# Kernel tuning notes

Measured on AMD Instinct MI355X. Metric: run time of the kernel, lower is better.

## Reference

```python
import jax, jax.numpy as jnp
import numpy as np

WINDOW_SIZE = 512  # init kwarg

def setup_inputs() -> dict:
    key = jax.random.key(0)
    kq, kk, kv = jax.random.split(key, 3)
    B, H, S, D = 1, 16, 4096, 64
    q = jax.random.normal(kq, (B, H, S, D), dtype=jnp.float32)
    k = jax.random.normal(kk, (B, H, S, D), dtype=jnp.float32)
    v = jax.random.normal(kv, (B, H, S, D), dtype=jnp.float32)
    return {"q": q, "k": k, "v": v}

def reference(q, k, v):
    # q,k,v: [B, H, S, D]
    B, H, S, D = q.shape
    scale = 1.0 / jnp.sqrt(jnp.asarray(D, dtype=q.dtype))
    scores = jnp.einsum('bhqd,bhkd->bhqk', q, k) * scale  # [B,H,S,S]
    # sliding-window band mask: token i attends to j in [i - w//2, i + w//2]
    idx = jnp.arange(S)
    band = jnp.abs(idx[:, None] - idx[None, :]) <= (WINDOW_SIZE // 2)  # [S,S]
    scores = jnp.where(band, scores, -jnp.inf)  # same as adding -inf mask
    probs = jax.nn.softmax(scores, axis=-1)
    return jnp.einsum('bhqk,bhkd->bhqd', probs, v)
```

## Files before the change

### kernel.cpp

```cpp
#include <hip/hip_runtime.h>
#include <math.h>

#define SEQ   4096
#define HD    64
#define NH    16
#define WHALF 256
#define QB    128
#define KT    64
#define KSTR  72
#define PLANE (KT * KSTR)

typedef __attribute__((ext_vector_type(8))) __bf16 bf16x8;
typedef __attribute__((ext_vector_type(8))) short short8v;
typedef __attribute__((ext_vector_type(4))) float f32x4;

__device__ __forceinline__ short bf16bits(float x) {
    __bf16 b = (__bf16)x;
    return __builtin_bit_cast(short, b);
}

#define MFMA32(A, B, C) __builtin_amdgcn_mfma_f32_16x16x32_bf16((A), (B), (C), 0, 0, 0)

#if __has_builtin(__builtin_amdgcn_exp2f)
#define EXP2F(x) __builtin_amdgcn_exp2f(x)
#else
#define EXP2F(x) __exp2f(x)
#endif

__global__ __launch_bounds__(512, 4)
void swa_mfma7_kernel(const float* __restrict__ q,
                      const float* __restrict__ k,
                      const float* __restrict__ v,
                      float* __restrict__ out) {
    __shared__ short smem[2 * 2 * PLANE];
    __shared__ short onesP[16 * KSTR];

    const int orig = blockIdx.x;
    const int work = ((orig & 7) << 6) + (orig >> 3);
    const int h    = work >> 5;
    const int q0   = (work & 31) * QB;

    const int t    = threadIdx.x;
    const int lane = t & 63;
    const int w    = t >> 6;
    const int n15  = lane & 15;
    const int g    = lane >> 4;
    const int qrow = q0 + w * 16 + n15;

    const float SCALE = 0.125f * 1.44269504088896340736f;

    for (int idx = t; idx < 16 * KSTR; idx += 512)
        onesP[idx] = (idx < KSTR) ? (short)0x3F80 : (short)0;

    bf16x8 qf[2];
    {
        const float* qp = q + ((size_t)h * SEQ + qrow) * HD;
        #pragma unroll
        for (int c = 0; c < 2; ++c) {
            const float4* p4 = reinterpret_cast<const float4*>(qp + 32 * c + 8 * g);
            float4 a = p4[0], b = p4[1];
            float xs[8] = {a.x, a.y, a.z, a.w, b.x, b.y, b.z, b.w};
            short8v q8;
            #pragma unroll
            for (int j = 0; j < 8; ++j) q8[j] = bf16bits(xs[j] * SCALE);
            qf[c] = __builtin_bit_cast(bf16x8, q8);
        }
    }

    f32x4 accO[4];
    #pragma unroll
    for (int dt = 0; dt < 4; ++dt) accO[dt] = (f32x4){0.f, 0.f, 0.f, 0.f};
    f32x4 accL = (f32x4){0.f, 0.f, 0.f, 0.f};

    int k0 = q0 - WHALF;           if (k0 < 0) k0 = 0;
    int k1 = q0 + QB - 1 + WHALF;  if (k1 > SEQ - 1) k1 = SEQ - 1;
    const int nt = (k1 + 1 - k0) >> 6;

    const int wqmin = q0 + w * 16;
    const int wqmax = wqmin + 15;
    const int wlo   = wqmin - WHALF;
    const int whi   = wqmax + WHALF;

    const float4* kb4 = reinterpret_cast<const float4*>(k + ((size_t)h * SEQ) * HD);
    const float*  vp  = v + ((size_t)h * SEQ) * HD;

    float4 kreg[2];
    float  vreg[8];

    #define LOADT(KTV)                                                       \
        {                                                                    \
            const int kt_ = (KTV);                                           \
            kreg[0] = kb4[(size_t)kt_ * 16 + t * 2 + 0];                     \
            kreg[1] = kb4[(size_t)kt_ * 16 + t * 2 + 1];                     \
            _Pragma("unroll")                                                \
            for (int j = 0; j < 8; ++j)                                      \
                vreg[j] = vp[(size_t)(kt_ + 8 * w + j) * HD + lane];         \
        }

    auto STAGE = [&](int b) {
        short* Kb = smem + b * 2 * PLANE;
        short* Vb = Kb + PLANE;

        const int p  = t >> 3;
        const int q5 = p & 31;
        const int R  = (p & 32) + (((q5 >> 2) & 1) << 4) + ((q5 >> 3) << 2) + (q5 & 3);

        const float* kf = reinterpret_cast<const float*>(&kreg[0]);
        short8v k8;
        #pragma unroll
        for (int j = 0; j < 8; ++j) k8[j] = bf16bits(kf[j]);
        *reinterpret_cast<short8v*>(&Kb[R * KSTR + (t & 7) * 8]) = k8;

        short8v v8;
        #pragma unroll
        for (int j = 0; j < 8; ++j) v8[j] = bf16bits(vreg[j]);
        *reinterpret_cast<short8v*>(&Vb[lane * KSTR + 8 * w]) = v8;
    };

    LOADT(k0);
    STAGE(0);
    if (nt > 1) LOADT(k0 + KT);
    __syncthreads();

    for (int i = 0; i < nt; ++i) {
        const int kt  = k0 + i * KT;
        const int cur = i & 1;

        if (i + 1 < nt) {
            STAGE(cur ^ 1);
            if (i + 2 < nt) LOADT(k0 + (i + 2) * KT);
        }

        const short* Kb = smem + cur * 2 * PLANE;
        const short* Vb = Kb + PLANE;

        #pragma unroll
        for (int kc = 0; kc < 2; ++kc) {
            const int cb = kt + kc * 32;
            if (cb > whi || cb + 31 < wlo) continue;

            f32x4 S[2];
            __builtin_amdgcn_s_setprio(1);
            #pragma unroll
            for (int s = 0; s < 2; ++s) {
                const int krow = (kc * 32 + s * 16 + n15) * KSTR + 8 * g;
                bf16x8 k0f = __builtin_bit_cast(bf16x8, *reinterpret_cast<const short8v*>(&Kb[krow]));
                bf16x8 k1f = __builtin_bit_cast(bf16x8, *reinterpret_cast<const short8v*>(&Kb[krow + 32]));
                f32x4 a = (f32x4){0.f, 0.f, 0.f, 0.f};
                a = MFMA32(k0f, qf[0], a);
                a = MFMA32(k1f, qf[1], a);
                S[s] = a;
            }
            __builtin_amdgcn_s_setprio(0);

            short8v p8s;
            const bool interior = (cb >= wqmax - WHALF) && (cb + 31 <= wqmin + WHALF);
            if (interior) {
                #pragma unroll
                for (int j = 0; j < 8; ++j)
                    p8s[j] = bf16bits(EXP2F(S[j >> 2][j & 3]));
            } else {
                const int kbase = cb + 8 * g;
                #pragma unroll
                for (int j = 0; j < 8; ++j) {
                    int key = kbase + j;
                    bool valid = (key >= qrow - WHALF) && (key <= qrow + WHALF);
                    float x = valid ? S[j >> 2][j & 3] : -1e30f;
                    p8s[j] = bf16bits(EXP2F(x));
                }
            }
            bf16x8 p8 = __builtin_bit_cast(bf16x8, p8s);

            __builtin_amdgcn_s_setprio(1);
            #pragma unroll
            for (int dt = 0; dt < 4; ++dt) {
                const int vrow = (dt * 16 + n15) * KSTR + kc * 32 + 8 * g;
                bf16x8 vf = __builtin_bit_cast(bf16x8, *reinterpret_cast<const short8v*>(&Vb[vrow]));
                accO[dt] = MFMA32(vf, p8, accO[dt]);
            }
            {
                bf16x8 of = __builtin_bit_cast(bf16x8,
                    *reinterpret_cast<const short8v*>(&onesP[n15 * KSTR + kc * 32 + 8 * g]));
                accL = MFMA32(of, p8, accL);
            }
            __builtin_amdgcn_s_setprio(0);
        }

        if (i + 1 < nt) __syncthreads();
    }

    const float lsum = __shfl(accL[0], n15);
    const float inv  = 1.0f / lsum;
    float* op = out + ((size_t)h * SEQ + qrow) * HD;
    #pragma unroll
    for (int dt = 0; dt < 4; ++dt) {
        *reinterpret_cast<f32x4*>(op + dt * 16 + 4 * g) = accO[dt] * inv;
    }
}

extern "C" void kernel_launch(void* const* d_in, const int* in_sizes, int n_in,
                              void* d_out, int out_size, void* d_ws, size_t ws_size,
                              hipStream_t stream) {
    const float* q = (const float*)d_in[0];
    const float* k = (const float*)d_in[1];
    const float* v = (const float*)d_in[2];
    float* out = (float*)d_out;

    dim3 grid(NH * (SEQ / QB));
    dim3 block(512);
    hipLaunchKernelGGL(swa_mfma7_kernel, grid, block, 0, stream, q, k, v, out);
}
```

Baseline: 27.97 us.

## Double query tile per block so each wave reuses K/V fragments for two row groups

```diff
diff --git a/kernel.cpp b/kernel.cpp
--- a/kernel.cpp
+++ b/kernel.cpp
@@ -5,7 +5,7 @@
 #define HD    64
 #define NH    16
 #define WHALF 256
-#define QB    128
+#define QB    256
 #define KT    64
 #define KSTR  72
 #define PLANE (KT * KSTR)
@@ -27,59 +27,73 @@
 #define EXP2F(x) __exp2f(x)
 #endif
 
-__global__ __launch_bounds__(512, 4)
-void swa_mfma7_kernel(const float* __restrict__ q,
+__global__ __launch_bounds__(512, 2)
+void swa_mfma8_kernel(const float* __restrict__ q,
                       const float* __restrict__ k,
                       const float* __restrict__ v,
                       float* __restrict__ out) {
     __shared__ short smem[2 * 2 * PLANE];
-    __shared__ short onesP[16 * KSTR];
 
     const int orig = blockIdx.x;
-    const int work = ((orig & 7) << 6) + (orig >> 3);
-    const int h    = work >> 5;
-    const int q0   = (work & 31) * QB;
+    const int work = ((orig & 7) << 5) | (orig >> 3);
+    const int h    = work >> 4;
+    const int q0   = (work & 15) * QB;
 
     const int t    = threadIdx.x;
     const int lane = t & 63;
     const int w    = t >> 6;
     const int n15  = lane & 15;
     const int g    = lane >> 4;
-    const int qrow = q0 + w * 16 + n15;
+
+    const int qa      = q0 + w * 32;
+    const int qrow_a  = qa + n15;
+    const int qrow_b  = qa + 16 + n15;
 
     const float SCALE = 0.125f * 1.44269504088896340736f;
 
-    for (int idx = t; idx < 16 * KSTR; idx += 512)
-        onesP[idx] = (idx < KSTR) ? (short)0x3F80 : (short)0;
-
-    bf16x8 qf[2];
+    bf16x8 qfa[2], qfb[2];
     {
-        const float* qp = q + ((size_t)h * SEQ + qrow) * HD;
+        const float* qpa = q + ((size_t)h * SEQ + qrow_a) * HD;
+        const float* qpb = q + ((size_t)h * SEQ + qrow_b) * HD;
         #pragma unroll
         for (int c = 0; c < 2; ++c) {
-            const float4* p4 = reinterpret_cast<const float4*>(qp + 32 * c + 8 * g);
-            float4 a = p4[0], b = p4[1];
-            float xs[8] = {a.x, a.y, a.z, a.w, b.x, b.y, b.z, b.w};
-            short8v q8;
+            const float4* pa4 = reinterpret_cast<const float4*>(qpa + 32 * c + 8 * g);
+            const float4* pb4 = reinterpret_cast<const float4*>(qpb + 32 * c + 8 * g);
+            float4 a0 = pa4[0], a1 = pa4[1], b0 = pb4[0], b1 = pb4[1];
+            float xa[8] = {a0.x, a0.y, a0.z, a0.w, a1.x, a1.y, a1.z, a1.w};
+            float xb[8] = {b0.x, b0.y, b0.z, b0.w, b1.x, b1.y, b1.z, b1.w};
+            short8v qa8, qb8;
             #pragma unroll
-            for (int j = 0; j < 8; ++j) q8[j] = bf16bits(xs[j] * SCALE);
-            qf[c] = __builtin_bit_cast(bf16x8, q8);
-        }
-    }
-
-    f32x4 accO[4];
+            for (int j = 0; j < 8; ++j) {
+                qa8[j] = bf16bits(xa[j] * SCALE);
+                qb8[j] = bf16bits(xb[j] * SCALE);
+            }
+            qfa[c] = __builtin_bit_cast(bf16x8, qa8);
+            qfb[c] = __builtin_bit_cast(bf16x8, qb8);
+        }
+    }
+
+    bf16x8 ones8;
+    {
+        short8v o8;
+        const short ov = (n15 == 0) ? (short)0x3F80 : (short)0;
+        #pragma unroll
+        for (int j = 0; j < 8; ++j) o8[j] = ov;
+        ones8 = __builtin_bit_cast(bf16x8, o8);
+    }
+
+    f32x4 accOa[4], accOb[4];
     #pragma unroll
-    for (int dt = 0; dt < 4; ++dt) accO[dt] = (f32x4){0.f, 0.f, 0.f, 0.f};
-    f32x4 accL = (f32x4){0.f, 0.f, 0.f, 0.f};
+    for (int dt = 0; dt < 4; ++dt) {
+        accOa[dt] = (f32x4){0.f, 0.f, 0.f, 0.f};
+        accOb[dt] = (f32x4){0.f, 0.f, 0.f, 0.f};
+    }
+    f32x4 accLa = (f32x4){0.f, 0.f, 0.f, 0.f};
+    f32x4 accLb = (f32x4){0.f, 0.f, 0.f, 0.f};
 
     int k0 = q0 - WHALF;           if (k0 < 0) k0 = 0;
     int k1 = q0 + QB - 1 + WHALF;  if (k1 > SEQ - 1) k1 = SEQ - 1;
     const int nt = (k1 + 1 - k0) >> 6;
-
-    const int wqmin = q0 + w * 16;
-    const int wqmax = wqmin + 15;
-    const int wlo   = wqmin - WHALF;
-    const int whi   = wqmax + WHALF;
 
     const float4* kb4 = reinterpret_cast<const float4*>(k + ((size_t)h * SEQ) * HD);
     const float*  vp  = v + ((size_t)h * SEQ) * HD;
@@ -137,64 +151,95 @@
         #pragma unroll
         for (int kc = 0; kc < 2; ++kc) {
             const int cb = kt + kc * 32;
-            if (cb > whi || cb + 31 < wlo) continue;
-
-            f32x4 S[2];
+            const bool aact = !(cb > qa + 15 + WHALF || cb + 31 < qa - WHALF);
+            const bool bact = !(cb > qa + 31 + WHALF || cb + 31 < qa + 16 - WHALF);
+            if (!aact && !bact) continue;
+
+            f32x4 Sa[2], Sb[2];
             __builtin_amdgcn_s_setprio(1);
             #pragma unroll
             for (int s = 0; s < 2; ++s) {
                 const int krow = (kc * 32 + s * 16 + n15) * KSTR + 8 * g;
                 bf16x8 k0f = __builtin_bit_cast(bf16x8, *reinterpret_cast<const short8v*>(&Kb[krow]));
                 bf16x8 k1f = __builtin_bit_cast(bf16x8, *reinterpret_cast<const short8v*>(&Kb[krow + 32]));
-                f32x4 a = (f32x4){0.f, 0.f, 0.f, 0.f};
-                a = MFMA32(k0f, qf[0], a);
-                a = MFMA32(k1f, qf[1], a);
-                S[s] = a;
+                if (aact) {
+                    f32x4 a = (f32x4){0.f, 0.f, 0.f, 0.f};
+                    a = MFMA32(k0f, qfa[0], a);
+                    a = MFMA32(k1f, qfa[1], a);
+                    Sa[s] = a;
+                }
+                if (bact) {
+                    f32x4 b = (f32x4){0.f, 0.f, 0.f, 0.f};
+                    b = MFMA32(k0f, qfb[0], b);
+                    b = MFMA32(k1f, qfb[1], b);
+                    Sb[s] = b;
+                }
             }
             __builtin_amdgcn_s_setprio(0);
 
-            short8v p8s;
-            const bool interior = (cb >= wqmax - WHALF) && (cb + 31 <= wqmin + WHALF);
-            if (interior) {
-                #pragma unroll
-                for (int j = 0; j < 8; ++j)
-                    p8s[j] = bf16bits(EXP2F(S[j >> 2][j & 3]));
-            } else {
-                const int kbase = cb + 8 * g;
-                #pragma unroll
-                for (int j = 0; j < 8; ++j) {
-                    int key = kbase + j;
-                    bool valid = (key >= qrow - WHALF) && (key <= qrow + WHALF);
-                    float x = valid ? S[j >> 2][j & 3] : -1e30f;
-                    p8s[j] = bf16bits(EXP2F(x));
-                }
-            }
-            bf16x8 p8 = __builtin_bit_cast(bf16x8, p8s);
+            const int kbase = cb + 8 * g;
+            bf16x8 pa8, pb8;
+            if (aact) {
+                short8v p8s;
+                const bool interior = (cb >= qa + 15 - WHALF) && (cb + 31 <= qa + WHALF);
+                if (interior) {
+                    #pragma unroll
+                    for (int j = 0; j < 8; ++j)
+                        p8s[j] = bf16bits(EXP2F(Sa[j >> 2][j & 3]));
+                } else {
+                    #pragma unroll
+                    for (int j = 0; j < 8; ++j) {
+                        int key = kbase + j;
+                        bool valid = (key >= qrow_a - WHALF) && (key <= qrow_a + WHALF);
+                        p8s[j] = bf16bits(EXP2F(valid ? Sa[j >> 2][j & 3] : -1e30f));
+                    }
+                }
+                pa8 = __builtin_bit_cast(bf16x8, p8s);
+            }
+            if (bact) {
+                short8v p8s;
+                const bool interior = (cb >= qa + 31 - WHALF) && (cb + 31 <= qa + 16 + WHALF);
+                if (interior) {
+                    #pragma unroll
+                    for (int j = 0; j < 8; ++j)
+                        p8s[j] = bf16bits(EXP2F(Sb[j >> 2][j & 3]));
+                } else {
+                    #pragma unroll
+                    for (int j = 0; j < 8; ++j) {
+                        int key = kbase + j;
+                        bool valid = (key >= qrow_b - WHALF) && (key <= qrow_b + WHALF);
+                        p8s[j] = bf16bits(EXP2F(valid ? Sb[j >> 2][j & 3] : -1e30f));
+                    }
+                }
+                pb8 = __builtin_bit_cast(bf16x8, p8s);
+            }
 
             __builtin_amdgcn_s_setprio(1);
             #pragma unroll
             for (int dt = 0; dt < 4; ++dt) {
                 const int vrow = (dt * 16 + n15) * KSTR + kc * 32 + 8 * g;
                 bf16x8 vf = __builtin_bit_cast(bf16x8, *reinterpret_cast<const short8v*>(&Vb[vrow]));
-                accO[dt] = MFMA32(vf, p8, accO[dt]);
-            }
-            {
-                bf16x8 of = __builtin_bit_cast(bf16x8,
-                    *reinterpret_cast<const short8v*>(&onesP[n15 * KSTR + kc * 32 + 8 * g]));
-                accL = MFMA32(of, p8, accL);
-            }
+                if (aact) accOa[dt] = MFMA32(vf, pa8, accOa[dt]);
+                if (bact) accOb[dt] = MFMA32(vf, pb8, accOb[dt]);
+            }
+            if (aact) accLa = MFMA32(ones8, pa8, accLa);
+            if (bact) accLb = MFMA32(ones8, pb8, accLb);
             __builtin_amdgcn_s_setprio(0);
         }
 
         if (i + 1 < nt) __syncthreads();
     }
 
-    const float lsum = __shfl(accL[0], n15);
-    const float inv  = 1.0f / lsum;
-    float* op = out + ((size_t)h * SEQ + qrow) * HD;
+    const float lsa = __shfl(accLa[0], n15);
+    const float lsb = __shfl(accLb[0], n15);
+    const float inva = 1.0f / lsa;
+    const float invb = 1.0f / lsb;
+    float* opa = out + ((size_t)h * SEQ + qrow_a) * HD;
+    float* opb = out + ((size_t)h * SEQ + qrow_b) * HD;
     #pragma unroll
     for (int dt = 0; dt < 4; ++dt) {
-        *reinterpret_cast<f32x4*>(op + dt * 16 + 4 * g) = accO[dt] * inv;
+        *reinterpret_cast<f32x4*>(opa + dt * 16 + 4 * g) = accOa[dt] * inva;
+        *reinterpret_cast<f32x4*>(opb + dt * 16 + 4 * g) = accOb[dt] * invb;
     }
 }
 
@@ -208,5 +253,5 @@
 
     dim3 grid(NH * (SEQ / QB));
     dim3 block(512);
-    hipLaunchKernelGGL(swa_mfma7_kernel, grid, block, 0, stream, q, k, v, out);
+    hipLaunchKernelGGL(swa_mfma8_kernel, grid, block, 0, stream, q, k, v, out);
 }
```

Result: slower. 33.05 us (+18.2%).

## Double key tile to 128 rows and keep ones-vector for row sums in registers

Applied to the files above, without the earlier changes.

```diff
diff --git a/kernel.cpp b/kernel.cpp
--- a/kernel.cpp
+++ b/kernel.cpp
@@ -6,9 +6,12 @@
 #define NH    16
 #define WHALF 256
 #define QB    128
-#define KT    64
+#define KT    128
 #define KSTR  72
-#define PLANE (KT * KSTR)
+#define VSTR  136
+#define KPLANE (KT * KSTR)
+#define VPLANE (HD * VSTR)
+#define BUFSZ  (KPLANE + VPLANE)
 
 typedef __attribute__((ext_vector_type(8))) __bf16 bf16x8;
 typedef __attribute__((ext_vector_type(8))) short short8v;
@@ -28,12 +31,11 @@
 #endif
 
 __global__ __launch_bounds__(512, 4)
-void swa_mfma7_kernel(const float* __restrict__ q,
-                      const float* __restrict__ k,
-                      const float* __restrict__ v,
-                      float* __restrict__ out) {
-    __shared__ short smem[2 * 2 * PLANE];
-    __shared__ short onesP[16 * KSTR];
+void swa_mfma10_kernel(const float* __restrict__ q,
+                       const float* __restrict__ k,
+                       const float* __restrict__ v,
+                       float* __restrict__ out) {
+    __shared__ short smem[2 * BUFSZ];
 
     const int orig = blockIdx.x;
     const int work = ((orig & 7) << 6) + (orig >> 3);
@@ -48,9 +50,6 @@
     const int qrow = q0 + w * 16 + n15;
 
     const float SCALE = 0.125f * 1.44269504088896340736f;
-
-    for (int idx = t; idx < 16 * KSTR; idx += 512)
-        onesP[idx] = (idx < KSTR) ? (short)0x3F80 : (short)0;
 
     bf16x8 qf[2];
     {
@@ -67,6 +66,15 @@
         }
     }
 
+    bf16x8 ones8;
+    {
+        short8v o8;
+        const short ov = (n15 == 0) ? (short)0x3F80 : (short)0;
+        #pragma unroll
+        for (int j = 0; j < 8; ++j) o8[j] = ov;
+        ones8 = __builtin_bit_cast(bf16x8, o8);
+    }
+
     f32x4 accO[4];
     #pragma unroll
     for (int dt = 0; dt < 4; ++dt) accO[dt] = (f32x4){0.f, 0.f, 0.f, 0.f};
@@ -74,7 +82,7 @@
 
     int k0 = q0 - WHALF;           if (k0 < 0) k0 = 0;
     int k1 = q0 + QB - 1 + WHALF;  if (k1 > SEQ - 1) k1 = SEQ - 1;
-    const int nt = (k1 + 1 - k0) >> 6;
+    const int nt = (k1 + 1 - k0) >> 7;
 
     const int wqmin = q0 + w * 16;
     const int wqmax = wqmin + 15;
@@ -84,37 +92,46 @@
     const float4* kb4 = reinterpret_cast<const float4*>(k + ((size_t)h * SEQ) * HD);
     const float*  vp  = v + ((size_t)h * SEQ) * HD;
 
-    float4 kreg[2];
-    float  vreg[8];
-
-    #define LOADT(KTV)                                                       \
-        {                                                                    \
-            const int kt_ = (KTV);                                           \
-            kreg[0] = kb4[(size_t)kt_ * 16 + t * 2 + 0];                     \
-            kreg[1] = kb4[(size_t)kt_ * 16 + t * 2 + 1];                     \
-            _Pragma("unroll")                                                \
-            for (int j = 0; j < 8; ++j)                                      \
-                vreg[j] = vp[(size_t)(kt_ + 8 * w + j) * HD + lane];         \
+    float4 kreg[4];
+    float  vreg[16];
+
+    #define LOADT(KTV)                                                        \
+        {                                                                     \
+            const int kt_ = (KTV);                                            \
+            _Pragma("unroll")                                                 \
+            for (int i = 0; i < 4; ++i)                                       \
+                kreg[i] = kb4[(size_t)kt_ * 16 + t * 4 + i];                  \
+            _Pragma("unroll")                                                 \
+            for (int j = 0; j < 16; ++j)                                      \
+                vreg[j] = vp[(size_t)(kt_ + 16 * w + j) * HD + lane];         \
         }
 
     auto STAGE = [&](int b) {
-        short* Kb = smem + b * 2 * PLANE;
-        short* Vb = Kb + PLANE;
-
-        const int p  = t >> 3;
+        short* Kb = smem + b * BUFSZ;
+        short* Vb = Kb + KPLANE;
+
+        const int p  = t >> 2;
         const int q5 = p & 31;
-        const int R  = (p & 32) + (((q5 >> 2) & 1) << 4) + ((q5 >> 3) << 2) + (q5 & 3);
+        const int R  = (p & 96) + (((q5 >> 2) & 1) << 4) + ((q5 >> 3) << 2) + (q5 & 3);
 
         const float* kf = reinterpret_cast<const float*>(&kreg[0]);
-        short8v k8;
-        #pragma unroll
-        for (int j = 0; j < 8; ++j) k8[j] = bf16bits(kf[j]);
-        *reinterpret_cast<short8v*>(&Kb[R * KSTR + (t & 7) * 8]) = k8;
-
-        short8v v8;
-        #pragma unroll
-        for (int j = 0; j < 8; ++j) v8[j] = bf16bits(vreg[j]);
-        *reinterpret_cast<short8v*>(&Vb[lane * KSTR + 8 * w]) = v8;
+        short8v k8a, k8b;
+        #pragma unroll
+        for (int j = 0; j < 8; ++j) {
+            k8a[j] = bf16bits(kf[j]);
+            k8b[j] = bf16bits(kf[8 + j]);
+        }
+        *reinterpret_cast<short8v*>(&Kb[R * KSTR + (t & 3) * 16])     = k8a;
+        *reinterpret_cast<short8v*>(&Kb[R * KSTR + (t & 3) * 16 + 8]) = k8b;
+
+        short8v v8a, v8b;
+        #pragma unroll
+        for (int j = 0; j < 8; ++j) {
+            v8a[j] = bf16bits(vreg[j]);
+            v8b[j] = bf16bits(vreg[8 + j]);
+        }
+        *reinterpret_cast<short8v*>(&Vb[lane * VSTR + 16 * w])     = v8a;
+        *reinterpret_cast<short8v*>(&Vb[lane * VSTR + 16 * w + 8]) = v8b;
     };
 
     LOADT(k0);
@@ -131,11 +148,11 @@
             if (i + 2 < nt) LOADT(k0 + (i + 2) * KT);
         }
 
-        const short* Kb = smem + cur * 2 * PLANE;
-        const short* Vb = Kb + PLANE;
-
-        #pragma unroll
-        for (int kc = 0; kc < 2; ++kc) {
+        const short* Kb = smem + cur * BUFSZ;
+        const short* Vb = Kb + KPLANE;
+
+        #pragma unroll
+        for (int kc = 0; kc < 4; ++kc) {
             const int cb = kt + kc * 32;
             if (cb > whi || cb + 31 < wlo) continue;
 
@@ -165,8 +182,7 @@
                 for (int j = 0; j < 8; ++j) {
                     int key = kbase + j;
                     bool valid = (key >= qrow - WHALF) && (key <= qrow + WHALF);
-                    float x = valid ? S[j >> 2][j & 3] : -1e30f;
-                    p8s[j] = bf16bits(EXP2F(x));
+                    p8s[j] = bf16bits(EXP2F(valid ? S[j >> 2][j & 3] : -1e30f));
                 }
             }
             bf16x8 p8 = __builtin_bit_cast(bf16x8, p8s);
@@ -174,15 +190,11 @@
             __builtin_amdgcn_s_setprio(1);
             #pragma unroll
             for (int dt = 0; dt < 4; ++dt) {
-                const int vrow = (dt * 16 + n15) * KSTR + kc * 32 + 8 * g;
+                const int vrow = (dt * 16 + n15) * VSTR + kc * 32 + 8 * g;
                 bf16x8 vf = __builtin_bit_cast(bf16x8, *reinterpret_cast<const short8v*>(&Vb[vrow]));
                 accO[dt] = MFMA32(vf, p8, accO[dt]);
             }
-            {
-                bf16x8 of = __builtin_bit_cast(bf16x8,
-                    *reinterpret_cast<const short8v*>(&onesP[n15 * KSTR + kc * 32 + 8 * g]));
-                accL = MFMA32(of, p8, accL);
-            }
+            accL = MFMA32(ones8, p8, accL);
             __builtin_amdgcn_s_setprio(0);
         }
 
@@ -208,5 +220,5 @@
 
     dim3 grid(NH * (SEQ / QB));
     dim3 block(512);
-    hipLaunchKernelGGL(swa_mfma7_kernel, grid, block, 0, stream, q, k, v, out);
+    hipLaunchKernelGGL(swa_mfma10_kernel, grid, block, 0, stream, q, k, v, out);
 }
```

After: 27.34 us. 2.2% less time.
